# Performance work log

Measured on AMD Instinct MI355X. Metric: run time of the kernel, lower is better.

Reference implementation:

```python
import jax, jax.numpy as jnp
import numpy as np

B, F, HDIM, HEADS = 256, 126, 256, 4
DH = HDIM // HEADS
N = F + 2                 # nodes per graph: [features..., user, item]
NT = B * N                # total nodes
E_PER_G = 2048
USER_NUM, ITEM_NUM, FEAT_NUM = 10000, 20000, 50000
NEG_SLOPE = 0.2


def setup_inputs() -> dict:
    key = jax.random.key(0)
    ks = jax.random.split(key, 16)
    fid = jax.random.randint(ks[0], (B * F,), 0, FEAT_NUM)
    userid = jax.random.randint(ks[1], (B,), 0, USER_NUM)
    itemid = jax.random.randint(ks[2], (B,), 0, ITEM_NUM)
    # random intra-graph edges, offset per graph
    src = jax.random.randint(ks[3], (B, E_PER_G), 0, N)
    dst = jax.random.randint(ks[4], (B, E_PER_G), 0, N)
    off = (jnp.arange(B) * N)[:, None]
    edge_index = jnp.stack([(src + off).reshape(-1), (dst + off).reshape(-1)])
    s = 0.05
    return {
        "fid": fid, "userid": userid, "itemid": itemid, "edge_index": edge_index,
        "feature_table": jax.random.normal(ks[5], (FEAT_NUM, HDIM)) * s,
        "user_table": jax.random.normal(ks[6], (USER_NUM, HDIM)) * s,
        "item_table": jax.random.normal(ks[7], (ITEM_NUM, HDIM)) * s,
        "W_feat": jax.random.normal(ks[8], (HDIM, HDIM)) * s,
        "W_user": jax.random.normal(ks[9], (HDIM, HDIM)) * s,
        "W_item": jax.random.normal(ks[10], (HDIM, HDIM)) * s,
        "W_gat": jax.random.normal(ks[11], (HDIM, HDIM)) * s,
        "a_src": jax.random.normal(ks[12], (HEADS, DH)) * s,
        "a_dst": jax.random.normal(ks[13], (HEADS, DH)) * s,
        "W_out": jax.random.normal(ks[14], (HDIM, 1)) * s,
        "b_out": jnp.zeros((1,)),
    }


def gat_layer(x, edge_index, W_gat, a_src, a_dst):
    # multi-head GAT with concat heads (GATNET, dropout disabled)
    n = x.shape[0]
    h = (x @ W_gat).reshape(n, HEADS, DH)            # [NT, H, DH]
    src, dst = edge_index[0], edge_index[1]
    alpha_s = jnp.einsum("nhd,hd->nh", h, a_src)      # [NT, H]
    alpha_d = jnp.einsum("nhd,hd->nh", h, a_dst)
    e = jax.nn.leaky_relu(alpha_s[src] + alpha_d[dst], NEG_SLOPE)  # [E, H]
    m = jax.ops.segment_max(e, dst, num_segments=n)
    m = jnp.where(jnp.isfinite(m), m, 0.0)
    ee = jnp.exp(e - m[dst])
    denom = jax.ops.segment_sum(ee, dst, num_segments=n)
    alpha = ee / (denom[dst] + 1e-16)                 # softmax over incoming edges
    msg = h[src] * alpha[:, :, None]                  # [E, H, DH]
    out = jax.ops.segment_sum(msg, dst, num_segments=n)
    return jax.nn.elu(out.reshape(n, HDIM))


def reference(fid, userid, itemid, edge_index, feature_table, user_table,
              item_table, W_feat, W_user, W_item, W_gat, a_src, a_dst,
              W_out, b_out):
    # embed + project node features
    f_node = feature_table[fid] @ W_feat              # [B*F, HDIM]
    u_node = user_table[userid] @ W_user              # [B, HDIM]
    i_node = item_table[itemid] @ W_item              # [B, HDIM]
    # per-graph concat [features, user, item] -> flat node matrix
    x = jnp.concatenate(
        [f_node.reshape(B, F, HDIM), u_node[:, None, :], i_node[:, None, :]],
        axis=1).reshape(NT, HDIM)
    hidden = gat_layer(x, edge_index, W_gat, a_src, a_dst)   # [NT, HDIM]
    # readout: feature nodes are the first F nodes of each graph
    hidden_f = hidden.reshape(B, N, HDIM)[:, :F].reshape(B * F, HDIM)
    logits_f = hidden_f @ W_out + b_out               # [B*F, 1]
    return logits_f
```

## Files before the change

kernel.cpp:

```cpp
#include <hip/hip_runtime.h>
#include <math.h>

#define F_ 126
#define NPG 128
#define EPG 2048
#define ET 524288
#define NEG_SLOPE 0.2f

typedef short bf16x8 __attribute__((ext_vector_type(8)));
typedef float f32x4 __attribute__((ext_vector_type(4)));

__device__ __forceinline__ float bf2f(unsigned short u) {
  return __uint_as_float(((unsigned)u) << 16);
}
__device__ __forceinline__ unsigned short f2bf(float f) {
  unsigned x = __float_as_uint(f);
  unsigned r = x + 0x7fffu + ((x >> 16) & 1u);
  return (unsigned short)(r >> 16);
}
__device__ __forceinline__ unsigned cvtpk(float lo, float hi) {
  unsigned r;
  asm("v_cvt_pk_bf16_f32 %0, %1, %2" : "=v"(r) : "v"(lo), "v"(hi));
  return r;
}
union bfpack { unsigned u[4]; bf16x8 v; };

#define SW(r)  (((r) & 7) << 4)
#define SWB(d) (((d) & 15) << 3)

#define WS_M    393216

__global__ __launch_bounds__(256) void k0p(
    const float* __restrict__ Wf, const float* __restrict__ Wu,
    const float* __restrict__ Wi, const float* __restrict__ Wg,
    const int* __restrict__ ei,
    unsigned short* __restrict__ wct, unsigned char* __restrict__ Mws) {
  const int blk = blockIdx.x;
  const int tid = threadIdx.x;
  if (blk < 96) {
    const int type = blk / 32;
    const int kc = blk % 32;
    const float* Wx = (type == 0) ? Wf : ((type == 1) ? Wu : Wi);
    __shared__ float Xs[8][256];
#pragma unroll
    for (int r = 0; r < 8; ++r) Xs[r][tid] = Wx[(kc * 8 + r) * 256 + tid];
    __syncthreads();
    float acc[8] = {};
#pragma unroll 16
    for (int j = 0; j < 256; ++j) {
      float wg = Wg[j * 256 + tid];
#pragma unroll
      for (int r = 0; r < 8; ++r) acc[r] += Xs[r][j] * wg;
    }
#pragma unroll
    for (int r = 0; r < 8; ++r)
      wct[((size_t)type * 256 + tid) * 256 + kc * 8 + r] = f2bf(acc[r]);
  } else {
    const int g = blk - 96;
    __shared__ __align__(16) unsigned char Ml[16384];
    {
      uint4 z = { 0, 0, 0, 0 };
#pragma unroll
      for (int i = 0; i < 4; ++i) *(uint4*)(Ml + tid * 16 + i * 4096) = z;
    }
    int4 sa = *(const int4*)(ei + (size_t)g * EPG + tid * 8);
    int4 sb = *(const int4*)(ei + (size_t)g * EPG + tid * 8 + 4);
    int4 da = *(const int4*)(ei + (size_t)ET + (size_t)g * EPG + tid * 8);
    int4 db = *(const int4*)(ei + (size_t)ET + (size_t)g * EPG + tid * 8 + 4);
    __syncthreads();
    int ss[8] = { sa.x - g * NPG, sa.y - g * NPG, sa.z - g * NPG, sa.w - g * NPG,
                  sb.x - g * NPG, sb.y - g * NPG, sb.z - g * NPG, sb.w - g * NPG };
    int dd[8] = { da.x - g * NPG, da.y - g * NPG, da.z - g * NPG, da.w - g * NPG,
                  db.x - g * NPG, db.y - g * NPG, db.z - g * NPG, db.w - g * NPG };
#pragma unroll
    for (int j = 0; j < 8; ++j) {
      int bofs = (dd[j] * 128 + ss[j]) ^ SWB(dd[j]);
      atomicAdd((int*)(Ml + (bofs & ~3)), 1 << ((bofs & 3) * 8));
    }
    __syncthreads();
    unsigned char* Mdst = Mws + (size_t)g * 16384;
#pragma unroll
    for (int i = 0; i < 4; ++i)
      *(uint4*)(Mdst + tid * 16 + i * 4096) = *(const uint4*)(Ml + tid * 16 + i * 4096);
  }
}

#define OFF_A    0
#define OFF_HT   0
#define OFF_M    65536
#define OFF_ES   81920
#define OFF_FS   83968
#define OFF_ED   86016
#define OFF_FD   88064
#define OFF_ASL  90112
#define OFF_ADL  91136
#define OFF_WO   92160
#define OFF_LP   93184
#define LDS_SZ   94208

__global__ __launch_bounds__(1024, 1) void k2f(
    const int* __restrict__ fid, const int* __restrict__ userid, const int* __restrict__ itemid,
    const float* __restrict__ ftab, const float* __restrict__ utab, const float* __restrict__ itab,
    const unsigned short* __restrict__ wct, const unsigned char* __restrict__ Mws,
    const float* __restrict__ a_src, const float* __restrict__ a_dst,
    const float* __restrict__ W_out, const float* __restrict__ b_out,
    float* __restrict__ out) {
  __shared__ __align__(16) char smem[LDS_SZ];
  const int g = blockIdx.x;
  const int tid = threadIdx.x;
  const int lane = tid & 63;
  const int wid = tid >> 6;
  const int rl = lane & 15;
  const int kg = lane >> 4;

  char* Ht = smem + OFF_HT;
  char* Mb = smem + OFF_M;
  float* EsT = (float*)(smem + OFF_ES);
  float* FsT = (float*)(smem + OFF_FS);
  float* EdT = (float*)(smem + OFF_ED);
  float* FdT = (float*)(smem + OFF_FD);
  float* asl = (float*)(smem + OFF_ASL);
  float* adl = (float*)(smem + OFF_ADL);
  float* wo  = (float*)(smem + OFF_WO);
  float* lpf = (float*)(smem + OFF_LP);

  *(uint4*)(Mb + tid * 16) = *(const uint4*)(Mws + (size_t)g * 16384 + tid * 16);

  if (tid < 256)      { asl[tid] = a_src[tid]; wo[tid] = W_out[tid]; }
  else if (tid < 512) { adl[tid - 256] = a_dst[tid - 256]; }
  const float bo = b_out[0];

  {
    const int r = tid >> 3, q = tid & 7;
    const float* srcrow;
    if (r < F_)       srcrow = ftab + (size_t)fid[g * F_ + r] * 256;
    else if (r == F_) srcrow = utab + (size_t)userid[g] * 256;
    else              srcrow = itab + (size_t)itemid[g] * 256;
    char* Ab = smem + OFF_A;
#pragma unroll
    for (int j = 0; j < 8; ++j) {
      float4 v = *(const float4*)(srcrow + q * 4 + j * 32);
      uint2 st;
      st.x = cvtpk(v.x, v.y);
      st.y = cvtpk(v.z, v.w);
      *(uint2*)(Ab + r * 512 + ((q * 8 + j * 64) ^ SW(r))) = st;
    }
  }
  __syncthreads();

  const int mh = wid & 3, nq = wid >> 2;
  const unsigned short* bp[4];
#pragma unroll
  for (int nf = 0; nf < 4; ++nf)
    bp[nf] = wct + (size_t)(nq * 64 + nf * 16 + rl) * 256;

  f32x4 acc[2][4] = {};
  {
    const char* Ab = smem + OFF_A;
#pragma unroll
    for (int ks = 0; ks < 8; ++ks) {
      bf16x8 af[2], bfv[4];
#pragma unroll
      for (int mf = 0; mf < 2; ++mf) {
        int row = mh * 32 + mf * 16 + rl;
        af[mf] = *(const bf16x8*)(Ab + row * 512 + ((ks * 64 + kg * 16) ^ SW(row)));
      }
#pragma unroll
      for (int nf = 0; nf < 4; ++nf)
        bfv[nf] = *(const bf16x8*)(bp[nf] + ks * 32 + kg * 8);
#pragma unroll
      for (int mf = 0; mf < 2; ++mf)
#pragma unroll
        for (int nf = 0; nf < 4; ++nf)
          acc[mf][nf] = __builtin_amdgcn_mfma_f32_16x16x32_bf16(af[mf], bfv[nf], acc[mf][nf], 0, 0, 0);
    }
  }

  {
    float asv[4], adv[4];
#pragma unroll
    for (int nf = 0; nf < 4; ++nf) {
      asv[nf] = asl[nq * 64 + nf * 16 + rl];
      adv[nf] = adl[nq * 64 + nf * 16 + rl];
    }
#pragma unroll
    for (int mf = 0; mf < 2; ++mf) {
#pragma unroll
      for (int i = 0; i < 4; ++i) {
        float ps = 0.f, pd = 0.f;
#pragma unroll
        for (int nf = 0; nf < 4; ++nf) { float v = acc[mf][nf][i]; ps += v * asv[nf]; pd += v * adv[nf]; }
#pragma unroll
        for (int d2 = 1; d2 < 16; d2 <<= 1) { ps += __shfl_xor(ps, d2); pd += __shfl_xor(pd, d2); }
        int row = mh * 32 + mf * 16 + kg * 4 + i;
        if (rl == 0 && row < F_) {
          EsT[nq * 128 + row] = __expf(ps);
          FsT[nq * 128 + row] = __expf(NEG_SLOPE * ps);
          EdT[nq * 128 + row] = __expf(pd);
          FdT[nq * 128 + row] = __expf(NEG_SLOPE * pd);
        }
      }
    }
  }
  __syncthreads();

  {
#pragma unroll
    for (int mf = 0; mf < 2; ++mf) {
      int srcb = mh * 32 + mf * 16 + kg * 4;
#pragma unroll
      for (int nf = 0; nf < 4; ++nf) {
        int dim = nq * 64 + nf * 16 + rl;
        unsigned lo = cvtpk(acc[mf][nf][0], acc[mf][nf][1]);
        unsigned hi = cvtpk(acc[mf][nf][2], acc[mf][nf][3]);
        int bofs = (dim * 256 + srcb * 2) ^ SW(dim);
        if (srcb < 124) { uint2 u = { lo, hi }; *(uint2*)(Ht + bofs) = u; }
        else            { *(unsigned*)(Ht + bofs) = lo; }
      }
    }
  }

  if (tid < 512) {
    const int r2 = F_ + (tid >> 8);
    const int c2 = tid & 255;
    const float* er = (tid < 256) ? (utab + (size_t)userid[g] * 256)
                                  : (itab + (size_t)itemid[g] * 256);
    const uint4* wr = (const uint4*)(wct + (size_t)(1 + (tid >> 8)) * 65536 + (size_t)c2 * 256);
    const float4* e4 = (const float4*)er;
    float hv = 0.f;
#pragma unroll 4
    for (int j = 0; j < 32; ++j) {
      uint4 w8 = wr[j];
      float4 e0 = e4[2 * j], e1 = e4[2 * j + 1];
      const unsigned short* wp = (const unsigned short*)&w8;
      hv += e0.x * bf2f(wp[0]) + e0.y * bf2f(wp[1]) + e0.z * bf2f(wp[2]) + e0.w * bf2f(wp[3]);
      hv += e1.x * bf2f(wp[4]) + e1.y * bf2f(wp[5]) + e1.z * bf2f(wp[6]) + e1.w * bf2f(wp[7]);
    }
    float gps = hv * asl[c2];
    float gpd = hv * adl[c2];
#pragma unroll
    for (int d2 = 32; d2 >= 1; d2 >>= 1) { gps += __shfl_xor(gps, d2); gpd += __shfl_xor(gpd, d2); }
    if (lane == 0) {
      int h2 = wid & 3;
      EsT[h2 * 128 + r2] = __expf(gps);
      FsT[h2 * 128 + r2] = __expf(NEG_SLOPE * gps);
      EdT[h2 * 128 + r2] = __expf(gpd);
      FdT[h2 * 128 + r2] = __expf(NEG_SLOPE * gpd);
    }
    *(unsigned short*)(Ht + ((c2 * 256 + r2 * 2) ^ SW(c2))) = f2bf(hv);
  }
  __syncthreads();

  float lp[4] = {};
  const int m2 = (wid & 7) * 16, n2 = (wid >> 3) * 32;
  const int drow = m2 + rl;

  for (int hd = 0; hd < 4; ++hd) {
    const float Edv = EdT[hd * 128 + drow];
    const float Fdv = FdT[hd * 128 + drow];
    float denp = 0.f;
    f32x4 acc2[2] = {};
#pragma unroll
    for (int ks = 0; ks < 4; ++ks) {
      uint2 m8 = *(const uint2*)(Mb + ((drow * 128 + ks * 32 + kg * 8) ^ SWB(drow)));
      f32x4 Es0 = *(const f32x4*)(&EsT[hd * 128 + ks * 32 + kg * 8]);
      f32x4 Es1 = *(const f32x4*)(&EsT[hd * 128 + ks * 32 + kg * 8 + 4]);
      f32x4 Fs0 = *(const f32x4*)(&FsT[hd * 128 + ks * 32 + kg * 8]);
      f32x4 Fs1 = *(const f32x4*)(&FsT[hd * 128 + ks * 32 + kg * 8 + 4]);
      float av[8];
#pragma unroll
      for (int j = 0; j < 8; ++j) {
        float mv = (float)(int)((j < 4 ? (m8.x >> (8 * j)) : (m8.y >> (8 * (j - 4)))) & 255u);
        float w = fmaxf(((j < 4) ? Es0[j] : Es1[j - 4]) * Edv,
                        ((j < 4) ? Fs0[j] : Fs1[j - 4]) * Fdv) * mv;
        av[j] = w;
        denp += w;
      }
      bfpack a2;
      a2.u[0] = cvtpk(av[0], av[1]); a2.u[1] = cvtpk(av[2], av[3]);
      a2.u[2] = cvtpk(av[4], av[5]); a2.u[3] = cvtpk(av[6], av[7]);
      bf16x8 b2[2];
#pragma unroll
      for (int nf = 0; nf < 2; ++nf) {
        int dim = hd * 64 + n2 + nf * 16 + rl;
        b2[nf] = *(const bf16x8*)(Ht + ((dim * 256 + ks * 64 + kg * 16) ^ SW(dim)));
      }
#pragma unroll
      for (int nf = 0; nf < 2; ++nf)
        acc2[nf] = __builtin_amdgcn_mfma_f32_16x16x32_bf16(a2.v, b2[nf], acc2[nf], 0, 0, 0);
    }
    denp += __shfl_xor(denp, 16);
    denp += __shfl_xor(denp, 32);
#pragma unroll
    for (int i = 0; i < 4; ++i) {
      float dni = __shfl(denp, kg * 4 + i);
      float rd = __builtin_amdgcn_rcpf(dni + 1e-16f);
#pragma unroll
      for (int nf = 0; nf < 2; ++nf) {
        float v = acc2[nf][i] * rd;
        v = (v > 0.f) ? v : (__expf(v) - 1.f);
        lp[i] += v * wo[hd * 64 + n2 + nf * 16 + rl];
      }
    }
  }

#pragma unroll
  for (int i = 0; i < 4; ++i) {
    float v = lp[i];
#pragma unroll
    for (int d2 = 1; d2 < 16; d2 <<= 1) v += __shfl_xor(v, d2);
    if (rl == 0) lpf[(m2 + kg * 4 + i) * 2 + (wid >> 3)] = v;
  }
  __syncthreads();
  if (tid < F_) out[(size_t)g * F_ + tid] = lpf[tid * 2] + lpf[tid * 2 + 1] + bo;
}

extern "C" void kernel_launch(void* const* d_in, const int* in_sizes, int n_in,
                              void* d_out, int out_size, void* d_ws, size_t ws_size,
                              hipStream_t stream) {
  const int* fid      = (const int*)d_in[0];
  const int* userid   = (const int*)d_in[1];
  const int* itemid   = (const int*)d_in[2];
  const int* ei       = (const int*)d_in[3];
  const float* ftab   = (const float*)d_in[4];
  const float* utab   = (const float*)d_in[5];
  const float* itab   = (const float*)d_in[6];
  const float* Wf     = (const float*)d_in[7];
  const float* Wu     = (const float*)d_in[8];
  const float* Wi     = (const float*)d_in[9];
  const float* Wg     = (const float*)d_in[10];
  const float* a_src  = (const float*)d_in[11];
  const float* a_dst  = (const float*)d_in[12];
  const float* W_out  = (const float*)d_in[13];
  const float* b_out  = (const float*)d_in[14];
  float* out = (float*)d_out;

  unsigned short* ws_wct = (unsigned short*)d_ws;
  unsigned char*  ws_M   = (unsigned char*)d_ws + WS_M;

  hipLaunchKernelGGL(k0p, dim3(352), dim3(256), 0, stream, Wf, Wu, Wi, Wg, ei, ws_wct, ws_M);
  hipLaunchKernelGGL(k2f, dim3(256), dim3(1024), 0, stream,
                     fid, userid, itemid, ftab, utab, itab, ws_wct, ws_M,
                     a_src, a_dst, W_out, b_out, out);
}
```

Before: 66.28 us.

## Stage combined weights through double-buffered LDS and compute user/item rows via MFMA

The fused GEMM now streams the combined weight matrix into a double-buffered LDS region in four K-chunks, with global loads for the next chunk overlapping MFMA rounds on the current one. This replaces per-wave direct global reads of the B operand. The scalar fp32 dot-product loop for the user and item rows is replaced by MFMA tiles on half of the waves, which take the relevant accumulator lane. LDS use rises to about 156 KB and three extra barriers are added, and the user/item MFMA still reads its weights straight from global memory.

```diff
diff --git a/kernel.cpp b/kernel.cpp
--- a/kernel.cpp
+++ b/kernel.cpp
@@ -87,16 +87,17 @@
 
 #define OFF_A    0
 #define OFF_HT   0
-#define OFF_M    65536
-#define OFF_ES   81920
-#define OFF_FS   83968
-#define OFF_ED   86016
-#define OFF_FD   88064
-#define OFF_ASL  90112
-#define OFF_ADL  91136
-#define OFF_WO   92160
-#define OFF_LP   93184
-#define LDS_SZ   94208
+#define OFF_B    65536
+#define OFF_M    131072
+#define OFF_ES   147456
+#define OFF_FS   149504
+#define OFF_ED   151552
+#define OFF_FD   153600
+#define OFF_ASL  155648
+#define OFF_ADL  156672
+#define OFF_WO   157696
+#define OFF_LP   158720
+#define LDS_SZ   159744
 
 __global__ __launch_bounds__(1024, 1) void k2f(
     const int* __restrict__ fid, const int* __restrict__ userid, const int* __restrict__ itemid,
@@ -130,6 +131,21 @@
   else if (tid < 512) { adl[tid - 256] = a_dst[tid - 256]; }
   const float bo = b_out[0];
 
+  const int bd = tid >> 2, bq = tid & 3;
+#define BSTAGE_LOAD(c, r0, r1)                                                   \
+  r0 = *(const uint4*)(wct + (size_t)bd * 256 + (c) * 64 + bq * 16);             \
+  r1 = *(const uint4*)(wct + (size_t)bd * 256 + (c) * 64 + bq * 16 + 8);
+#define BSTAGE_WRITE(c, r0, r1)                                                  \
+  { char* Bw = smem + OFF_B + ((c) & 1) * 32768;                                 \
+    *(uint4*)(Bw + bd * 128 + ((bq * 32) ^ SW(bd))) = r0;                        \
+    *(uint4*)(Bw + bd * 128 + ((bq * 32 + 16) ^ SW(bd))) = r1; }
+
+  {
+    uint4 s0, s1;
+    BSTAGE_LOAD(0, s0, s1)
+    BSTAGE_WRITE(0, s0, s1)
+  }
+
   {
     const int r = tid >> 3, q = tid & 7;
     const float* srcrow;
@@ -149,32 +165,52 @@
   __syncthreads();
 
   const int mh = wid & 3, nq = wid >> 2;
-  const unsigned short* bp[4];
-#pragma unroll
-  for (int nf = 0; nf < 4; ++nf)
-    bp[nf] = wct + (size_t)(nq * 64 + nf * 16 + rl) * 256;
-
   f32x4 acc[2][4] = {};
-  {
-    const char* Ab = smem + OFF_A;
-#pragma unroll
-    for (int ks = 0; ks < 8; ++ks) {
-      bf16x8 af[2], bfv[4];
-#pragma unroll
-      for (int mf = 0; mf < 2; ++mf) {
-        int row = mh * 32 + mf * 16 + rl;
-        af[mf] = *(const bf16x8*)(Ab + row * 512 + ((ks * 64 + kg * 16) ^ SW(row)));
-      }
-#pragma unroll
-      for (int nf = 0; nf < 4; ++nf)
-        bfv[nf] = *(const bf16x8*)(bp[nf] + ks * 32 + kg * 8);
-#pragma unroll
-      for (int mf = 0; mf < 2; ++mf)
-#pragma unroll
-        for (int nf = 0; nf < 4; ++nf)
-          acc[mf][nf] = __builtin_amdgcn_mfma_f32_16x16x32_bf16(af[mf], bfv[nf], acc[mf][nf], 0, 0, 0);
-    }
-  }
+
+#define G1ROUND(buf, ks)                                                                   \
+  {                                                                                        \
+    const char* Ab = smem + OFF_A;                                                         \
+    const char* Bc = smem + OFF_B + (buf) * 32768;                                         \
+    bf16x8 af[2], bfv[4];                                                                  \
+    _Pragma("unroll")                                                                      \
+    for (int mf = 0; mf < 2; ++mf) {                                                       \
+      int row = mh * 32 + mf * 16 + rl;                                                    \
+      af[mf] = *(const bf16x8*)(Ab + row * 512 + (((ks) * 64 + kg * 16) ^ SW(row)));       \
+    }                                                                                      \
+    _Pragma("unroll")                                                                      \
+    for (int nf = 0; nf < 4; ++nf) {                                                       \
+      int d = nq * 64 + nf * 16 + rl;                                                      \
+      bfv[nf] = *(const bf16x8*)(Bc + d * 128 + ((((ks) & 1) * 64 + kg * 16) ^ SW(d)));    \
+    }                                                                                      \
+    _Pragma("unroll")                                                                      \
+    for (int mf = 0; mf < 2; ++mf)                                                         \
+      _Pragma("unroll")                                                                    \
+      for (int nf = 0; nf < 4; ++nf)                                                       \
+        acc[mf][nf] = __builtin_amdgcn_mfma_f32_16x16x32_bf16(af[mf], bfv[nf], acc[mf][nf], 0, 0, 0); \
+  }
+
+  {
+    uint4 s0, s1;
+    BSTAGE_LOAD(1, s0, s1)
+    G1ROUND(0, 0) G1ROUND(0, 1)
+    BSTAGE_WRITE(1, s0, s1)
+  }
+  __syncthreads();
+  {
+    uint4 s0, s1;
+    BSTAGE_LOAD(2, s0, s1)
+    G1ROUND(1, 2) G1ROUND(1, 3)
+    BSTAGE_WRITE(2, s0, s1)
+  }
+  __syncthreads();
+  {
+    uint4 s0, s1;
+    BSTAGE_LOAD(3, s0, s1)
+    G1ROUND(0, 4) G1ROUND(0, 5)
+    BSTAGE_WRITE(3, s0, s1)
+  }
+  __syncthreads();
+  G1ROUND(1, 6) G1ROUND(1, 7)
 
   {
     float asv[4], adv[4];
@@ -202,6 +238,49 @@
       }
     }
   }
+
+  float ghv0 = 0.f, ghv1 = 0.f, ghv2 = 0.f, ghv3 = 0.f;
+  int gr2 = 126, gdg = 0, gt = 1;
+  if (wid >= 8) {
+    const int w = wid - 8;
+    gt = 1 + (w & 1);
+    gdg = w >> 1;
+    gr2 = 125 + gt;
+    const unsigned short* bgp[4];
+#pragma unroll
+    for (int nf = 0; nf < 4; ++nf)
+      bgp[nf] = wct + (size_t)(gt * 256 + gdg * 64 + nf * 16 + rl) * 256;
+    f32x4 acc2[4] = {};
+    const char* Ab = smem + OFF_A;
+#pragma unroll
+    for (int ks = 0; ks < 8; ++ks) {
+      int row = 112 + rl;
+      bf16x8 af = *(const bf16x8*)(Ab + row * 512 + ((ks * 64 + kg * 16) ^ SW(row)));
+      bf16x8 bfv[4];
+#pragma unroll
+      for (int nf = 0; nf < 4; ++nf)
+        bfv[nf] = *(const bf16x8*)(bgp[nf] + ks * 32 + kg * 8);
+#pragma unroll
+      for (int nf = 0; nf < 4; ++nf)
+        acc2[nf] = __builtin_amdgcn_mfma_f32_16x16x32_bf16(af, bfv[nf], acc2[nf], 0, 0, 0);
+    }
+    ghv0 = (gt == 1) ? acc2[0][2] : acc2[0][3];
+    ghv1 = (gt == 1) ? acc2[1][2] : acc2[1][3];
+    ghv2 = (gt == 1) ? acc2[2][2] : acc2[2][3];
+    ghv3 = (gt == 1) ? acc2[3][2] : acc2[3][3];
+    float ps = ghv0 * asl[gdg * 64 + rl] + ghv1 * asl[gdg * 64 + 16 + rl]
+             + ghv2 * asl[gdg * 64 + 32 + rl] + ghv3 * asl[gdg * 64 + 48 + rl];
+    float pd = ghv0 * adl[gdg * 64 + rl] + ghv1 * adl[gdg * 64 + 16 + rl]
+             + ghv2 * adl[gdg * 64 + 32 + rl] + ghv3 * adl[gdg * 64 + 48 + rl];
+#pragma unroll
+    for (int d2 = 1; d2 < 16; d2 <<= 1) { ps += __shfl_xor(ps, d2); pd += __shfl_xor(pd, d2); }
+    if (kg == 3 && rl == 0) {
+      EsT[gdg * 128 + gr2] = __expf(ps);
+      FsT[gdg * 128 + gr2] = __expf(NEG_SLOPE * ps);
+      EdT[gdg * 128 + gr2] = __expf(pd);
+      FdT[gdg * 128 + gr2] = __expf(NEG_SLOPE * pd);
+    }
+  }
   __syncthreads();
 
   {
@@ -218,36 +297,16 @@
         else            { *(unsigned*)(Ht + bofs) = lo; }
       }
     }
-  }
-
-  if (tid < 512) {
-    const int r2 = F_ + (tid >> 8);
-    const int c2 = tid & 255;
-    const float* er = (tid < 256) ? (utab + (size_t)userid[g] * 256)
-                                  : (itab + (size_t)itemid[g] * 256);
-    const uint4* wr = (const uint4*)(wct + (size_t)(1 + (tid >> 8)) * 65536 + (size_t)c2 * 256);
-    const float4* e4 = (const float4*)er;
-    float hv = 0.f;
-#pragma unroll 4
-    for (int j = 0; j < 32; ++j) {
-      uint4 w8 = wr[j];
-      float4 e0 = e4[2 * j], e1 = e4[2 * j + 1];
-      const unsigned short* wp = (const unsigned short*)&w8;
-      hv += e0.x * bf2f(wp[0]) + e0.y * bf2f(wp[1]) + e0.z * bf2f(wp[2]) + e0.w * bf2f(wp[3]);
-      hv += e1.x * bf2f(wp[4]) + e1.y * bf2f(wp[5]) + e1.z * bf2f(wp[6]) + e1.w * bf2f(wp[7]);
-    }
-    float gps = hv * asl[c2];
-    float gpd = hv * adl[c2];
-#pragma unroll
-    for (int d2 = 32; d2 >= 1; d2 >>= 1) { gps += __shfl_xor(gps, d2); gpd += __shfl_xor(gpd, d2); }
-    if (lane == 0) {
-      int h2 = wid & 3;
-      EsT[h2 * 128 + r2] = __expf(gps);
-      FsT[h2 * 128 + r2] = __expf(NEG_SLOPE * gps);
-      EdT[h2 * 128 + r2] = __expf(gpd);
-      FdT[h2 * 128 + r2] = __expf(NEG_SLOPE * gpd);
-    }
-    *(unsigned short*)(Ht + ((c2 * 256 + r2 * 2) ^ SW(c2))) = f2bf(hv);
+    if (wid >= 8 && kg == 3) {
+      int d0 = gdg * 64 + rl;
+      *(unsigned short*)(Ht + ((d0 * 256 + gr2 * 2) ^ SW(d0))) = f2bf(ghv0);
+      int d1 = d0 + 16;
+      *(unsigned short*)(Ht + ((d1 * 256 + gr2 * 2) ^ SW(d1))) = f2bf(ghv1);
+      int d2 = d0 + 32;
+      *(unsigned short*)(Ht + ((d2 * 256 + gr2 * 2) ^ SW(d2))) = f2bf(ghv2);
+      int d3 = d0 + 48;
+      *(unsigned short*)(Ht + ((d3 * 256 + gr2 * 2) ^ SW(d3))) = f2bf(ghv3);
+    }
   }
   __syncthreads();
 
```

Measured after the change: 53.36 us (median of 2 runs). -19.5%, faster.
